# Kernel optimization log

Hardware: AMD Instinct MI355X
Metric: run time of the kernel (lower is better)

The kernel has to match this reference:

```python
import jax, jax.numpy as jnp
import numpy as np

EPS = 1e-12  # F.normalize eps

def _l2norm(v):
    n = jnp.sqrt(jnp.sum(v * v, axis=-1, keepdims=True))
    return v / jnp.maximum(n, EPS)

def setup_inputs() -> dict:
    key = jax.random.key(0)
    k1, k2, k3 = jax.random.split(key, 3)
    B, C, H, Wd = 32, 256, 64, 64
    M = 64
    x = jax.random.normal(k1, (B, C, H, Wd), dtype=jnp.float32)
    stdv = 1.0 / np.sqrt(M)
    W = jax.random.uniform(k2, (M, C), dtype=jnp.float32, minval=-stdv, maxval=stdv)
    label_batch = jax.random.randint(k3, (B,), 0, 2)
    return {"x": x, "W": W, "label_batch": label_batch}

def reference(x, W, label_batch):
    B, C, H, Wd = x.shape
    M = W.shape[0]
    # [B, HW, C] tokens; key == query == flattened input (pos=False)
    tok = x.transpose(0, 2, 3, 1).reshape(B, H * Wd, C)
    # per-pixel contribution to each prototype, softmax over pixels (dim=1)
    proto_weight = jax.nn.softmax(jnp.einsum('bnc,mc->bnm', tok, W), axis=1)
    # prototypes [B, M, C], L2-normalized
    proto = _l2norm(jnp.einsum('bnm,bnc->bmc', proto_weight, tok))
    # relevance of each pixel to each prototype, softmax over prototypes
    score = jax.nn.softmax(jnp.einsum('bnc,bmc->bnm', tok, proto), axis=-1)
    # reconstructed query
    new_query = _l2norm(jnp.einsum('bnm,bmc->bnc', score, proto))
    # compact loss: MSE(keys, nearest prototype) (new_cpt == 'True')
    top1 = jnp.argmax(score, axis=-1)                      # [B, HW]
    pos = jnp.take_along_axis(proto, top1[:, :, None], axis=1)  # [B, HW, C]
    compact_loss = jnp.mean((tok - pos) ** 2)
    # distance loss: push prototypes apart
    p2 = jnp.sum(proto * proto, axis=-1)                   # [B, M]
    sqd = p2[:, :, None] + p2[:, None, :] - 2.0 * jnp.einsum('bmc,bkc->bmk', proto, proto)
    dis = 1.0 - sqd
    dis = dis * (dis > 0).astype(dis.dtype)
    dis = jnp.triu(dis, k=1)
    dis_loss = jnp.mean(jnp.sum(dis, axis=(1, 2)) * 2.0 / (M * (M - 1)))
    out = new_query.transpose(0, 2, 1).reshape(B, C, H, Wd)
    return (out, compact_loss, dis_loss)
```

## Files before the change

kernel.cpp:

```cpp
#include <hip/hip_runtime.h>
#include <math.h>

#define B 32
#define C 256
#define M 64
#define N 4096

typedef __attribute__((ext_vector_type(8))) short s16x8;
typedef __attribute__((ext_vector_type(8))) __bf16 bf16x8;
typedef __attribute__((ext_vector_type(4))) float f32x4;
typedef __attribute__((ext_vector_type(4))) unsigned short u16x4;
typedef __attribute__((ext_vector_type(8))) unsigned short u16x8;

static constexpr float EPS = 1e-12f;

__device__ __forceinline__ unsigned short f2bf(float f) {
    unsigned u = __float_as_uint(f);
    u += 0x7FFFu + ((u >> 16) & 1u);
    return (unsigned short)(u >> 16);
}
__device__ __forceinline__ float bf2f(unsigned short h) {
    return __uint_as_float((unsigned)h << 16);
}
__device__ __forceinline__ f32x4 MFMA(s16x8 a, s16x8 b, f32x4 c) {
    return __builtin_amdgcn_mfma_f32_16x16x32_bf16(
        __builtin_bit_cast(bf16x8, a), __builtin_bit_cast(bf16x8, b), c, 0, 0, 0);
}
__device__ __forceinline__ s16x8 cvt8(const f32x4 a, const f32x4 b) {
    bf16x8 h;
    h[0] = (__bf16)a[0]; h[1] = (__bf16)a[1]; h[2] = (__bf16)a[2]; h[3] = (__bf16)a[3];
    h[4] = (__bf16)b[0]; h[5] = (__bf16)b[1]; h[6] = (__bf16)b[2]; h[7] = (__bf16)b[3];
    return __builtin_bit_cast(s16x8, h);
}
__device__ __forceinline__ int swz(int n) {
    return (((n >> 2) & 3) | ((n & 1) << 2)) << 3;
}

__global__ __launch_bounds__(256) void kW_convert(const float* __restrict__ Wf,
                                                  unsigned short* __restrict__ Wb) {
    const int i = blockIdx.x * 256 + threadIdx.x;
    Wb[i] = f2bf(Wf[i]);
}

__global__ __launch_bounds__(256) void k01(const float* __restrict__ x,
                                           const unsigned short* __restrict__ Wb,
                                           unsigned short* __restrict__ xbt,
                                           unsigned short* __restrict__ Sb,
                                           float* __restrict__ xsq) {
    const int nb = blockIdx.x, b = blockIdx.y;
    const int t = threadIdx.x;
    __shared__ unsigned short tsT[64 * 256];
    __shared__ float xred[16][68];
    const int g = t & 15, cp = t >> 4;
    float part[4] = {0.f, 0.f, 0.f, 0.f};
    const float* xrow = x + (size_t)b * C * N + (size_t)nb * 64 + 4 * g;
#pragma unroll
    for (int i = 0; i < 16; ++i) {
        const int c = cp + 16 * i;
        const f32x4 q = *(const f32x4*)(xrow + (size_t)c * N);
#pragma unroll
        for (int k = 0; k < 4; ++k) {
            const float v = q[k];
            part[k] += v * v;
            const int n = 4 * g + k;
            tsT[n * 256 + (c ^ swz(n))] = f2bf(v);
        }
    }
#pragma unroll
    for (int k = 0; k < 4; ++k) xred[cp][4 * g + k] = part[k];
    __syncthreads();
    if (t < 64) {
        float s = 0.f;
#pragma unroll
        for (int j = 0; j < 16; ++j) s += xred[j][t];
        xsq[(size_t)b * N + nb * 64 + t] = s;
    }
    {
        const int l = t & 31, nh = t >> 5;
#pragma unroll
        for (int j = 0; j < 8; ++j) {
            const int n = nh + 8 * j;
            const int c0 = l * 8;
            const u16x8 v = *(const u16x8*)(&tsT[n * 256 + (c0 ^ swz(n))]);
            *(u16x8*)(xbt + ((size_t)b * N + nb * 64 + n) * C + c0) = v;
        }
    }
    const int wv = t >> 6, lane = t & 63, li = lane & 15, lk = lane >> 4;
    const f32x4 zv = {0.f, 0.f, 0.f, 0.f};
    f32x4 acc[4] = {zv, zv, zv, zv};
    const unsigned short* br = Wb + (size_t)(wv * 16 + li) * C + lk * 8;
#pragma unroll
    for (int c0 = 0; c0 < C; c0 += 32) {
        const s16x8 bfrag = *(const s16x8*)(br + c0);
#pragma unroll
        for (int s = 0; s < 4; ++s) {
            const int n = s * 16 + li;
            const s16x8 a = *(const s16x8*)(&tsT[n * 256 + ((lk * 8 + c0) ^ swz(n))]);
            acc[s] = MFMA(a, bfrag, acc[s]);
        }
    }
    unsigned short* Srow = Sb + ((size_t)b * M + wv * 16 + li) * N + nb * 64;
#pragma unroll
    for (int s = 0; s < 4; ++s) {
        u16x4 h;
#pragma unroll
        for (int r = 0; r < 4; ++r) h[r] = f2bf(acc[s][r]);
        *(u16x4*)(Srow + s * 16 + lk * 4) = h;
    }
}

__global__ __launch_bounds__(256) void k2_softmax_n(const unsigned short* __restrict__ Sb,
                                                    unsigned short* __restrict__ Pb) {
    const int m = blockIdx.x, b = blockIdx.y;
    const unsigned short* col = Sb + ((size_t)b * M + m) * N;
    unsigned short* po = Pb + ((size_t)b * M + m) * N;
    const int t = threadIdx.x;
    float v[16];
    const u16x8 h0 = *(const u16x8*)(col + t * 16);
    const u16x8 h1 = *(const u16x8*)(col + t * 16 + 8);
#pragma unroll
    for (int i = 0; i < 8; ++i) v[i] = bf2f(h0[i]);
#pragma unroll
    for (int i = 0; i < 8; ++i) v[8 + i] = bf2f(h1[i]);
    float mx = -INFINITY;
#pragma unroll
    for (int i = 0; i < 16; ++i) mx = fmaxf(mx, v[i]);
#pragma unroll
    for (int off = 32; off >= 1; off >>= 1) mx = fmaxf(mx, __shfl_xor(mx, off));
    __shared__ float redm[4], reds[4];
    const int wave = t >> 6, lane = t & 63;
    if (lane == 0) redm[wave] = mx;
    __syncthreads();
    mx = fmaxf(fmaxf(redm[0], redm[1]), fmaxf(redm[2], redm[3]));
    float s = 0.f;
#pragma unroll
    for (int i = 0; i < 16; ++i) {
        v[i] = __expf(v[i] - mx);
        s += v[i];
    }
#pragma unroll
    for (int off = 32; off >= 1; off >>= 1) s += __shfl_xor(s, off);
    if (lane == 0) reds[wave] = s;
    __syncthreads();
    s = reds[0] + reds[1] + reds[2] + reds[3];
    const float inv = 1.f / s;
    u16x8 o0, o1;
#pragma unroll
    for (int i = 0; i < 8; ++i) o0[i] = f2bf(v[i] * inv);
#pragma unroll
    for (int i = 0; i < 8; ++i) o1[i] = f2bf(v[8 + i] * inv);
    *(u16x8*)(po + t * 16) = o0;
    *(u16x8*)(po + t * 16 + 8) = o1;
}

__global__ __launch_bounds__(256) void k3_mfma(const float* __restrict__ x,
                                               const unsigned short* __restrict__ Pb,
                                               float* __restrict__ parts) {
    const int ck = blockIdx.x, b = blockIdx.y;
    const int wv = threadIdx.x >> 6, lane = threadIdx.x & 63;
    const int li = lane & 15, lk = lane >> 4;
    const int c0w = wv * 64;
    const int nb = ck * 512;
    const f32x4 zv = {0.f, 0.f, 0.f, 0.f};
    f32x4 acc[4][4];
#pragma unroll
    for (int s = 0; s < 4; ++s)
#pragma unroll
        for (int u = 0; u < 4; ++u) acc[s][u] = zv;
    const float* ar = x + ((size_t)b * C + c0w + li) * N + nb + lk * 8;
    const unsigned short* br = Pb + ((size_t)b * M + li) * N + nb + lk * 8;
#pragma unroll 4
    for (int n0 = 0; n0 < 512; n0 += 32) {
        s16x8 af[4], bf_[4];
#pragma unroll
        for (int s = 0; s < 4; ++s) {
            const float* p = ar + (size_t)(s * 16) * N + n0;
            af[s] = cvt8(*(const f32x4*)p, *(const f32x4*)(p + 4));
        }
#pragma unroll
        for (int u = 0; u < 4; ++u) bf_[u] = *(const s16x8*)(br + (size_t)(u * 16) * N + n0);
#pragma unroll
        for (int s = 0; s < 4; ++s)
#pragma unroll
            for (int u = 0; u < 4; ++u) acc[s][u] = MFMA(af[s], bf_[u], acc[s][u]);
    }
    float* pp = parts + ((size_t)b * 8 + ck) * M * C;
#pragma unroll
    for (int s = 0; s < 4; ++s)
#pragma unroll
        for (int u = 0; u < 4; ++u)
            *(f32x4*)(pp + (size_t)(u * 16 + li) * C + c0w + s * 16 + lk * 4) = acc[s][u];
}

__global__ __launch_bounds__(256) void k3b_reduce(const float* __restrict__ parts,
                                                  unsigned short* __restrict__ proto_bf,
                                                  unsigned short* __restrict__ protoT_bf,
                                                  float* __restrict__ p2) {
    const int mb = blockIdx.x, b = blockIdx.y;
    const int t = threadIdx.x;
    const int ml = t >> 5, cl = t & 31;
    const int m = mb * 8 + ml;
    const int c0 = cl * 8;
    float v[8] = {0.f, 0.f, 0.f, 0.f, 0.f, 0.f, 0.f, 0.f};
    const float* pbase = parts + (size_t)b * 8 * M * C + (size_t)m * C + c0;
#pragma unroll
    for (int ck = 0; ck < 8; ++ck) {
        const f32x4 q0 = *(const f32x4*)(pbase + (size_t)ck * M * C);
        const f32x4 q1 = *(const f32x4*)(pbase + (size_t)ck * M * C + 4);
#pragma unroll
        for (int j = 0; j < 4; ++j) { v[j] += q0[j]; v[4 + j] += q1[j]; }
    }
    float sq = 0.f;
#pragma unroll
    for (int j = 0; j < 8; ++j) sq += v[j] * v[j];
#pragma unroll
    for (int off = 16; off >= 1; off >>= 1) sq += __shfl_xor(sq, off);
    const float denom = fmaxf(sqrtf(sq), EPS);
    const float scale = 1.f / denom;
    if (cl == 0) p2[b * M + m] = sq / (denom * denom);
    u16x8 h;
#pragma unroll
    for (int j = 0; j < 8; ++j) h[j] = f2bf(v[j] * scale);
    *(u16x8*)(proto_bf + ((size_t)b * M + m) * C + c0) = h;
#pragma unroll
    for (int j = 0; j < 8; ++j)
        protoT_bf[((size_t)b * C + c0 + j) * M + m] = h[j];
}

__global__ __launch_bounds__(256) void k4_score(const unsigned short* __restrict__ proto_bf,
                                                const unsigned short* __restrict__ xbt,
                                                const float* __restrict__ p2,
                                                const float* __restrict__ xsq,
                                                unsigned short* __restrict__ pnm,
                                                float* __restrict__ cparts) {
    const int b = blockIdx.y;
    const int wv = threadIdx.x >> 6, lane = threadIdx.x & 63;
    const int li = lane & 15, lk = lane >> 4;
    const int nbase = blockIdx.x * 256 + wv * 64;
    const f32x4 zv = {0.f, 0.f, 0.f, 0.f};
    f32x4 acc[4][4];
#pragma unroll
    for (int s = 0; s < 4; ++s)
#pragma unroll
        for (int u = 0; u < 4; ++u) acc[s][u] = zv;
    const unsigned short* ar = proto_bf + ((size_t)b * M + li) * C + lk * 8;
    const unsigned short* br = xbt + ((size_t)b * N + nbase + li) * C + lk * 8;
#pragma unroll
    for (int c0 = 0; c0 < C; c0 += 32) {
        s16x8 af[4], bf_[4];
#pragma unroll
        for (int s = 0; s < 4; ++s) af[s] = *(const s16x8*)(ar + (size_t)(s * 16) * C + c0);
#pragma unroll
        for (int u = 0; u < 4; ++u) bf_[u] = *(const s16x8*)(br + (size_t)(u * 16) * C + c0);
#pragma unroll
        for (int s = 0; s < 4; ++s)
#pragma unroll
            for (int u = 0; u < 4; ++u) acc[s][u] = MFMA(af[s], bf_[u], acc[s][u]);
    }
    float csum = 0.f;
#pragma unroll
    for (int u = 0; u < 4; ++u) {
        const int n = nbase + u * 16 + li;
        float vmax = -INFINITY;
#pragma unroll
        for (int s = 0; s < 4; ++s)
#pragma unroll
            for (int r = 0; r < 4; ++r) vmax = fmaxf(vmax, acc[s][u][r]);
        vmax = fmaxf(vmax, __shfl_xor(vmax, 16));
        vmax = fmaxf(vmax, __shfl_xor(vmax, 32));
        int t1 = 1 << 30;
#pragma unroll
        for (int s = 0; s < 4; ++s)
#pragma unroll
            for (int r = 0; r < 4; ++r)
                if (acc[s][u][r] == vmax) t1 = min(t1, s * 16 + lk * 4 + r);
        t1 = min(t1, __shfl_xor(t1, 16));
        t1 = min(t1, __shfl_xor(t1, 32));
        float es = 0.f;
#pragma unroll
        for (int s = 0; s < 4; ++s)
#pragma unroll
            for (int r = 0; r < 4; ++r) {
                const float e = __expf(acc[s][u][r] - vmax);
                acc[s][u][r] = e;
                es += e;
            }
        es += __shfl_xor(es, 16);
        es += __shfl_xor(es, 32);
        const float inv = 1.f / es;
        unsigned short* prow = pnm + ((size_t)b * N + n) * M;
#pragma unroll
        for (int s = 0; s < 4; ++s) {
            u16x4 h;
#pragma unroll
            for (int r = 0; r < 4; ++r) h[r] = f2bf(acc[s][u][r] * inv);
            *(u16x4*)(prow + s * 16 + lk * 4) = h;
        }
        if (lk == 0) csum += xsq[(size_t)b * N + n] - 2.f * vmax + p2[b * M + t1];
    }
#pragma unroll
    for (int off = 32; off >= 1; off >>= 1) csum += __shfl_xor(csum, off);
    __shared__ float red[4];
    if (lane == 0) red[wv] = csum;
    __syncthreads();
    if (threadIdx.x == 0)
        cparts[b * 16 + blockIdx.x] = red[0] + red[1] + red[2] + red[3];
}

__global__ __launch_bounds__(256) void k4b_mfma(const unsigned short* __restrict__ pnm,
                                                const unsigned short* __restrict__ protoT_bf,
                                                float* __restrict__ out) {
    const int b = blockIdx.y;
    const int wv = threadIdx.x >> 6, lane = threadIdx.x & 63;
    const int li = lane & 15, lk = lane >> 4;
    const int n0 = blockIdx.x * 64;
    const int cb = wv * 64;
    const f32x4 zv = {0.f, 0.f, 0.f, 0.f};
    f32x4 acc[4][4];
#pragma unroll
    for (int s = 0; s < 4; ++s)
#pragma unroll
        for (int u = 0; u < 4; ++u) acc[s][u] = zv;
    const unsigned short* ar = pnm + ((size_t)b * N + n0 + li) * M + lk * 8;
    const unsigned short* br = protoT_bf + ((size_t)b * C + cb + li) * M + lk * 8;
#pragma unroll
    for (int m0 = 0; m0 < M; m0 += 32) {
        s16x8 af[4], bf_[4];
#pragma unroll
        for (int s = 0; s < 4; ++s) af[s] = *(const s16x8*)(ar + (size_t)(s * 16) * M + m0);
#pragma unroll
        for (int u = 0; u < 4; ++u) bf_[u] = *(const s16x8*)(br + (size_t)(u * 16) * M + m0);
#pragma unroll
        for (int s = 0; s < 4; ++s)
#pragma unroll
            for (int u = 0; u < 4; ++u) acc[s][u] = MFMA(af[s], bf_[u], acc[s][u]);
    }
    __shared__ float ls[4][64];
    __shared__ float ls2[64];
    float psq[4][4];
#pragma unroll
    for (int s = 0; s < 4; ++s)
#pragma unroll
        for (int r = 0; r < 4; ++r) {
            float sum = 0.f;
#pragma unroll
            for (int u = 0; u < 4; ++u) sum += acc[s][u][r] * acc[s][u][r];
#pragma unroll
            for (int off = 8; off >= 1; off >>= 1) sum += __shfl_xor(sum, off);
            psq[s][r] = sum;
        }
    if (li == 0) {
#pragma unroll
        for (int s = 0; s < 4; ++s)
#pragma unroll
            for (int r = 0; r < 4; ++r) ls[wv][s * 16 + lk * 4 + r] = psq[s][r];
    }
    __syncthreads();
    if (threadIdx.x < 64) {
        const int tt = threadIdx.x;
        const float tot = ls[0][tt] + ls[1][tt] + ls[2][tt] + ls[3][tt];
        ls2[tt] = 1.f / fmaxf(sqrtf(tot), EPS);
    }
    __syncthreads();
    float scl[4][4];
#pragma unroll
    for (int s = 0; s < 4; ++s)
#pragma unroll
        for (int r = 0; r < 4; ++r) scl[s][r] = ls2[s * 16 + lk * 4 + r];
    float* ob = out + (size_t)b * C * N;
#pragma unroll
    for (int s = 0; s < 4; ++s)
#pragma unroll
        for (int u = 0; u < 4; ++u) {
            f32x4 q;
#pragma unroll
            for (int r = 0; r < 4; ++r) q[r] = acc[s][u][r] * scl[s][r];
            *(f32x4*)(ob + (size_t)(cb + u * 16 + li) * N + n0 + s * 16 + lk * 4) = q;
        }
}

__global__ __launch_bounds__(256) void k5_dis(const unsigned short* __restrict__ proto_bf,
                                              const float* __restrict__ p2,
                                              float* __restrict__ dparts) {
    const int q = blockIdx.x;
    const int b = blockIdx.y;
    const unsigned short* pr = proto_bf + (size_t)b * M * C;
    __shared__ float pl[M * C];
    for (int idx = threadIdx.x; idx < M * C; idx += 256) {
        int m = idx >> 8, c = idx & 255;
        pl[m * 256 + (c ^ (m & 31))] = bf2f(pr[idx]);
    }
    __syncthreads();
    float sum = 0.f;
    for (int k = 0; k < 2; ++k) {
        const int pair = q * 512 + k * 256 + threadIdx.x;
        const int i = pair >> 6, j = pair & 63;
        if (j > i) {
            float g = 0.f;
#pragma unroll 8
            for (int c = 0; c < C; ++c)
                g += pl[i * 256 + (c ^ (i & 31))] * pl[j * 256 + (c ^ (j & 31))];
            const float d = 1.f - (p2[b * M + i] + p2[b * M + j] - 2.f * g);
            sum += fmaxf(d, 0.f);
        }
    }
#pragma unroll
    for (int off = 32; off >= 1; off >>= 1) sum += __shfl_xor(sum, off);
    __shared__ float red[4];
    const int wave = threadIdx.x >> 6, lane = threadIdx.x & 63;
    if (lane == 0) red[wave] = sum;
    __syncthreads();
    if (threadIdx.x == 0) dparts[b * 8 + q] = red[0] + red[1] + red[2] + red[3];
}

__global__ __launch_bounds__(256) void k6_final(const float* __restrict__ cparts,
                                                const float* __restrict__ dparts,
                                                float* __restrict__ losses) {
    const int t = threadIdx.x;
    float cs = cparts[t] + cparts[t + 256];
    float ds = dparts[t];
#pragma unroll
    for (int off = 32; off >= 1; off >>= 1) {
        cs += __shfl_xor(cs, off);
        ds += __shfl_xor(ds, off);
    }
    __shared__ float rc[4], rd[4];
    const int wave = t >> 6, lane = t & 63;
    if (lane == 0) { rc[wave] = cs; rd[wave] = ds; }
    __syncthreads();
    if (t == 0) {
        const float ctot = rc[0] + rc[1] + rc[2] + rc[3];
        const float dtot = rd[0] + rd[1] + rd[2] + rd[3];
        losses[0] = ctot / ((float)B * (float)N * (float)C);
        losses[1] = dtot * (2.f / (float)(M * (M - 1))) / (float)B;
    }
}

extern "C" void kernel_launch(void* const* d_in, const int* in_sizes, int n_in,
                              void* d_out, int out_size, void* d_ws, size_t ws_size,
                              hipStream_t stream) {
    const float* x = (const float*)d_in[0];
    const float* Wf = (const float*)d_in[1];
    float* out = (float*)d_out;

    unsigned short* xbt = (unsigned short*)d_out;
    float* losses = out + (size_t)B * C * N;

    float* wsf = (float*)d_ws;
    unsigned short* Sbf = (unsigned short*)wsf;
    float* parts = wsf;
    unsigned short* Pbf = (unsigned short*)(wsf + 4194304);
    unsigned short* pnm = Pbf;
    float* xsq = wsf + 8388608;
    unsigned short* proto_bf = (unsigned short*)(wsf + 8519680);
    unsigned short* protoT_bf = (unsigned short*)(wsf + 8781824);
    unsigned short* Wb = (unsigned short*)(wsf + 9043968);
    float* p2 = wsf + 9052160;
    float* cparts = wsf + 9054208;
    float* dparts = wsf + 9054720;

    kW_convert<<<dim3(64), 256, 0, stream>>>(Wf, Wb);
    k01<<<dim3(N / 64, B), 256, 0, stream>>>(x, Wb, xbt, Sbf, xsq);
    k2_softmax_n<<<dim3(M, B), 256, 0, stream>>>(Sbf, Pbf);
    k3_mfma<<<dim3(8, B), 256, 0, stream>>>(x, Pbf, parts);
    k3b_reduce<<<dim3(8, B), 256, 0, stream>>>(parts, proto_bf, protoT_bf, p2);
    k4_score<<<dim3(N / 256, B), 256, 0, stream>>>(proto_bf, xbt, p2, xsq, pnm, cparts);
    k4b_mfma<<<dim3(N / 64, B), 256, 0, stream>>>(pnm, protoT_bf, out);
    k5_dis<<<dim3(8, B), 256, 0, stream>>>(proto_bf, p2, dparts);
    k6_final<<<1, 256, 0, stream>>>(cparts, dparts, losses);
}
```

Measured before the change: 178.0 us.

## Fold W conversion into k01, vectorize LDS transpose, drop redundant score normalization

Removes the separate W-to-bf16 conversion kernel; k01 now reads W in fp32 and converts the fragments inline. The k01 transpose loads four channels per thread and writes packed 4-element bf16 stores to shared memory instead of scalar stores. Manual round-to-nearest bf16 conversion is replaced with the native __bf16 cast throughout. The per-pixel softmax in k4_score skips the sum and reciprocal because the later L2 normalization cancels any per-row scale; the unnormalized exponentials can be larger, which is harmless within bf16 range.

```diff
diff --git a/kernel.cpp b/kernel.cpp
--- a/kernel.cpp
+++ b/kernel.cpp
@@ -8,16 +8,16 @@
 
 typedef __attribute__((ext_vector_type(8))) short s16x8;
 typedef __attribute__((ext_vector_type(8))) __bf16 bf16x8;
+typedef __attribute__((ext_vector_type(4))) __bf16 bf16x4;
 typedef __attribute__((ext_vector_type(4))) float f32x4;
 typedef __attribute__((ext_vector_type(4))) unsigned short u16x4;
 typedef __attribute__((ext_vector_type(8))) unsigned short u16x8;
 
 static constexpr float EPS = 1e-12f;
 
-__device__ __forceinline__ unsigned short f2bf(float f) {
-    unsigned u = __float_as_uint(f);
-    u += 0x7FFFu + ((u >> 16) & 1u);
-    return (unsigned short)(u >> 16);
+__device__ __forceinline__ unsigned short b16(float f) {
+    __bf16 h = (__bf16)f;
+    return __builtin_bit_cast(unsigned short, h);
 }
 __device__ __forceinline__ float bf2f(unsigned short h) {
     return __uint_as_float((unsigned)h << 16);
@@ -36,14 +36,8 @@
     return (((n >> 2) & 3) | ((n & 1) << 2)) << 3;
 }
 
-__global__ __launch_bounds__(256) void kW_convert(const float* __restrict__ Wf,
-                                                  unsigned short* __restrict__ Wb) {
-    const int i = blockIdx.x * 256 + threadIdx.x;
-    Wb[i] = f2bf(Wf[i]);
-}
-
 __global__ __launch_bounds__(256) void k01(const float* __restrict__ x,
-                                           const unsigned short* __restrict__ Wb,
+                                           const float* __restrict__ Wf,
                                            unsigned short* __restrict__ xbt,
                                            unsigned short* __restrict__ Sb,
                                            float* __restrict__ xsq) {
@@ -51,23 +45,29 @@
     const int t = threadIdx.x;
     __shared__ unsigned short tsT[64 * 256];
     __shared__ float xred[16][68];
-    const int g = t & 15, cp = t >> 4;
+    const int nq = t & 15, cq = t >> 4;
     float part[4] = {0.f, 0.f, 0.f, 0.f};
-    const float* xrow = x + (size_t)b * C * N + (size_t)nb * 64 + 4 * g;
-#pragma unroll
-    for (int i = 0; i < 16; ++i) {
-        const int c = cp + 16 * i;
-        const f32x4 q = *(const f32x4*)(xrow + (size_t)c * N);
+    const float* xrow = x + (size_t)b * C * N + (size_t)nb * 64 + 4 * nq;
+#pragma unroll
+    for (int step = 0; step < 4; ++step) {
+        const int c0 = cq * 4 + step * 64;
+        f32x4 q[4];
+#pragma unroll
+        for (int i = 0; i < 4; ++i) q[i] = *(const f32x4*)(xrow + (size_t)(c0 + i) * N);
 #pragma unroll
         for (int k = 0; k < 4; ++k) {
-            const float v = q[k];
-            part[k] += v * v;
-            const int n = 4 * g + k;
-            tsT[n * 256 + (c ^ swz(n))] = f2bf(v);
-        }
-    }
-#pragma unroll
-    for (int k = 0; k < 4; ++k) xred[cp][4 * g + k] = part[k];
+            const int n = 4 * nq + k;
+            bf16x4 hb;
+#pragma unroll
+            for (int i = 0; i < 4; ++i) {
+                part[k] += q[i][k] * q[i][k];
+                hb[i] = (__bf16)q[i][k];
+            }
+            *(u16x4*)(&tsT[n * 256 + (c0 ^ swz(n))]) = __builtin_bit_cast(u16x4, hb);
+        }
+    }
+#pragma unroll
+    for (int k = 0; k < 4; ++k) xred[cq][4 * nq + k] = part[k];
     __syncthreads();
     if (t < 64) {
         float s = 0.f;
@@ -88,10 +88,10 @@
     const int wv = t >> 6, lane = t & 63, li = lane & 15, lk = lane >> 4;
     const f32x4 zv = {0.f, 0.f, 0.f, 0.f};
     f32x4 acc[4] = {zv, zv, zv, zv};
-    const unsigned short* br = Wb + (size_t)(wv * 16 + li) * C + lk * 8;
+    const float* wr = Wf + (size_t)(wv * 16 + li) * C + lk * 8;
 #pragma unroll
     for (int c0 = 0; c0 < C; c0 += 32) {
-        const s16x8 bfrag = *(const s16x8*)(br + c0);
+        const s16x8 bfrag = cvt8(*(const f32x4*)(wr + c0), *(const f32x4*)(wr + c0 + 4));
 #pragma unroll
         for (int s = 0; s < 4; ++s) {
             const int n = s * 16 + li;
@@ -102,10 +102,10 @@
     unsigned short* Srow = Sb + ((size_t)b * M + wv * 16 + li) * N + nb * 64;
 #pragma unroll
     for (int s = 0; s < 4; ++s) {
-        u16x4 h;
-#pragma unroll
-        for (int r = 0; r < 4; ++r) h[r] = f2bf(acc[s][r]);
-        *(u16x4*)(Srow + s * 16 + lk * 4) = h;
+        bf16x4 h;
+#pragma unroll
+        for (int r = 0; r < 4; ++r) h[r] = (__bf16)acc[s][r];
+        *(u16x4*)(Srow + s * 16 + lk * 4) = __builtin_bit_cast(u16x4, h);
     }
 }
 
@@ -144,13 +144,13 @@
     __syncthreads();
     s = reds[0] + reds[1] + reds[2] + reds[3];
     const float inv = 1.f / s;
-    u16x8 o0, o1;
-#pragma unroll
-    for (int i = 0; i < 8; ++i) o0[i] = f2bf(v[i] * inv);
-#pragma unroll
-    for (int i = 0; i < 8; ++i) o1[i] = f2bf(v[8 + i] * inv);
-    *(u16x8*)(po + t * 16) = o0;
-    *(u16x8*)(po + t * 16 + 8) = o1;
+    bf16x8 o0, o1;
+#pragma unroll
+    for (int i = 0; i < 8; ++i) o0[i] = (__bf16)(v[i] * inv);
+#pragma unroll
+    for (int i = 0; i < 8; ++i) o1[i] = (__bf16)(v[8 + i] * inv);
+    *(u16x8*)(po + t * 16) = __builtin_bit_cast(u16x8, o0);
+    *(u16x8*)(po + t * 16 + 8) = __builtin_bit_cast(u16x8, o1);
 }
 
 __global__ __launch_bounds__(256) void k3_mfma(const float* __restrict__ x,
@@ -218,13 +218,14 @@
     const float denom = fmaxf(sqrtf(sq), EPS);
     const float scale = 1.f / denom;
     if (cl == 0) p2[b * M + m] = sq / (denom * denom);
-    u16x8 h;
-#pragma unroll
-    for (int j = 0; j < 8; ++j) h[j] = f2bf(v[j] * scale);
-    *(u16x8*)(proto_bf + ((size_t)b * M + m) * C + c0) = h;
+    bf16x8 h;
+#pragma unroll
+    for (int j = 0; j < 8; ++j) h[j] = (__bf16)(v[j] * scale);
+    const u16x8 hu = __builtin_bit_cast(u16x8, h);
+    *(u16x8*)(proto_bf + ((size_t)b * M + m) * C + c0) = hu;
 #pragma unroll
     for (int j = 0; j < 8; ++j)
-        protoT_bf[((size_t)b * C + c0 + j) * M + m] = h[j];
+        protoT_bf[((size_t)b * C + c0 + j) * M + m] = hu[j];
 }
 
 __global__ __launch_bounds__(256) void k4_score(const unsigned short* __restrict__ proto_bf,
@@ -276,25 +277,13 @@
                 if (acc[s][u][r] == vmax) t1 = min(t1, s * 16 + lk * 4 + r);
         t1 = min(t1, __shfl_xor(t1, 16));
         t1 = min(t1, __shfl_xor(t1, 32));
-        float es = 0.f;
-#pragma unroll
-        for (int s = 0; s < 4; ++s)
-#pragma unroll
-            for (int r = 0; r < 4; ++r) {
-                const float e = __expf(acc[s][u][r] - vmax);
-                acc[s][u][r] = e;
-                es += e;
-            }
-        es += __shfl_xor(es, 16);
-        es += __shfl_xor(es, 32);
-        const float inv = 1.f / es;
         unsigned short* prow = pnm + ((size_t)b * N + n) * M;
 #pragma unroll
         for (int s = 0; s < 4; ++s) {
-            u16x4 h;
-#pragma unroll
-            for (int r = 0; r < 4; ++r) h[r] = f2bf(acc[s][u][r] * inv);
-            *(u16x4*)(prow + s * 16 + lk * 4) = h;
+            bf16x4 h;
+#pragma unroll
+            for (int r = 0; r < 4; ++r) h[r] = (__bf16)__expf(acc[s][u][r] - vmax);
+            *(u16x4*)(prow + s * 16 + lk * 4) = __builtin_bit_cast(u16x4, h);
         }
         if (lk == 0) csum += xsq[(size_t)b * N + n] - 2.f * vmax + p2[b * M + t1];
     }
@@ -413,11 +402,12 @@
     if (threadIdx.x == 0) dparts[b * 8 + q] = red[0] + red[1] + red[2] + red[3];
 }
 
-__global__ __launch_bounds__(256) void k6_final(const float* __restrict__ cparts,
+__global__ __launch_bounds__(256) void k6_final(const float* __restrict__ cparts, int ncp,
                                                 const float* __restrict__ dparts,
                                                 float* __restrict__ losses) {
     const int t = threadIdx.x;
-    float cs = cparts[t] + cparts[t + 256];
+    float cs = 0.f;
+    for (int i = t; i < ncp; i += 256) cs += cparts[i];
     float ds = dparts[t];
 #pragma unroll
     for (int off = 32; off >= 1; off >>= 1) {
@@ -442,11 +432,10 @@
     const float* x = (const float*)d_in[0];
     const float* Wf = (const float*)d_in[1];
     float* out = (float*)d_out;
+    float* wsf = (float*)d_ws;
+    float* losses = out + (size_t)B * C * N;
 
     unsigned short* xbt = (unsigned short*)d_out;
-    float* losses = out + (size_t)B * C * N;
-
-    float* wsf = (float*)d_ws;
     unsigned short* Sbf = (unsigned short*)wsf;
     float* parts = wsf;
     unsigned short* Pbf = (unsigned short*)(wsf + 4194304);
@@ -454,18 +443,16 @@
     float* xsq = wsf + 8388608;
     unsigned short* proto_bf = (unsigned short*)(wsf + 8519680);
     unsigned short* protoT_bf = (unsigned short*)(wsf + 8781824);
-    unsigned short* Wb = (unsigned short*)(wsf + 9043968);
     float* p2 = wsf + 9052160;
     float* cparts = wsf + 9054208;
     float* dparts = wsf + 9054720;
 
-    kW_convert<<<dim3(64), 256, 0, stream>>>(Wf, Wb);
-    k01<<<dim3(N / 64, B), 256, 0, stream>>>(x, Wb, xbt, Sbf, xsq);
+    k01<<<dim3(N / 64, B), 256, 0, stream>>>(x, Wf, xbt, Sbf, xsq);
     k2_softmax_n<<<dim3(M, B), 256, 0, stream>>>(Sbf, Pbf);
     k3_mfma<<<dim3(8, B), 256, 0, stream>>>(x, Pbf, parts);
     k3b_reduce<<<dim3(8, B), 256, 0, stream>>>(parts, proto_bf, protoT_bf, p2);
     k4_score<<<dim3(N / 256, B), 256, 0, stream>>>(proto_bf, xbt, p2, xsq, pnm, cparts);
     k4b_mfma<<<dim3(N / 64, B), 256, 0, stream>>>(pnm, protoT_bf, out);
     k5_dis<<<dim3(8, B), 256, 0, stream>>>(proto_bf, p2, dparts);
-    k6_final<<<1, 256, 0, stream>>>(cparts, dparts, losses);
-}
+    k6_final<<<1, 256, 0, stream>>>(cparts, B * 16, dparts, losses);
+}
```

Measured after the change: 173.4 us. 1.03x faster.
